# Kernel tuning notes

Hardware: AMD Instinct MI355X
Metric: run time of the kernel (lower is better)

The kernel has to match this reference:

```python
import jax, jax.numpy as jnp
import numpy as np

B, T = 1024, 8192
NUM_WORDS = 2048  # ph2word.max() + 1, forced by construction in setup_inputs
OFFSET = 1.0
LAMBDA_P, LAMBDA_W, LAMBDA_S = 0.6, 0.3, 0.1
RULES_SCALE = 0.3
INIT_TOKENS = np.array([94, 122, 100, 92, 43, 27], dtype=np.int32)
INIT_DURS = np.array([2.0, 3.0, 2.0, 2.0, 5.0, 5.0], dtype=np.float32)
RATIO_TOKENS = np.array([44, 28, 29, 27, 121, 43], dtype=np.int32)


def setup_inputs() -> dict:
    key = jax.random.key(0)
    k1, k2, k3, k4 = jax.random.split(key, 4)
    dur_pred = jax.random.uniform(k1, (B, T), dtype=jnp.float32) * 10.0
    dur_gt = jax.random.uniform(k2, (B, T), dtype=jnp.float32) * 10.0
    ph2word = jnp.sort(jax.random.randint(k3, (B, T), 0, NUM_WORDS, dtype=jnp.int32), axis=1)
    ph2word = ph2word.at[:, -1].set(NUM_WORDS - 1)  # guarantee max == NUM_WORDS-1 (static shape)
    txt_tokens = jax.random.randint(k4, (B, T), 0, 150, dtype=jnp.int32)
    return {"dur_pred": dur_pred, "dur_gt": dur_gt, "ph2word": ph2word, "txt_tokens": txt_tokens}


def _linear2log(x):
    return jnp.log(x + OFFSET)


def _mse(a, b):
    d = a - b
    return jnp.mean(d * d)


def _dur_rules(dur_pred, txt_tokens):
    # Vectorized form of the sequential double loop. At step i the carry value
    # dur_rules[:, i] is unconditionally reset to dur_pred[:, i], so the ratio
    # rule's forward write to i+1 never survives; final value is
    #   dur_pred[i] - self_adjust(i) + neighbor_gaps_from(i+1).
    tok = txt_tokens[..., None]  # [B,T,1]
    in_init = jnp.any(tok == jnp.asarray(INIT_TOKENS), axis=-1)
    expected = jnp.sum(jnp.where(tok == jnp.asarray(INIT_TOKENS), jnp.asarray(INIT_DURS), 0.0), axis=-1)
    gap1 = dur_pred - expected
    fire1 = in_init & (gap1 > 0)
    gap1 = jnp.where(fire1, gap1, 0.0)

    in_ratio = jnp.any(tok == jnp.asarray(RATIO_TOKENS), axis=-1)
    dp_next = jnp.concatenate([dur_pred[:, 1:], jnp.zeros_like(dur_pred[:, :1])], axis=1)
    valid_next = jnp.arange(dur_pred.shape[1]) < dur_pred.shape[1] - 1
    fire2 = in_ratio & valid_next[None, :] & (3.0 * dur_pred > dp_next)
    gap2 = jnp.where(fire2, dur_pred - dp_next / 3.0, 0.0)

    # ratio rule overwrites (not adds to) the self position when it fires
    self_adj = jnp.where(fire2, gap2, jnp.where(fire1, gap1, 0.0))
    dur_rules = dur_pred - self_adj
    # gaps from iteration i+1 are added to position i (only for i+1 >= 1, always true)
    dur_rules = dur_rules.at[:, :-1].add((gap1 + gap2)[:, 1:])
    return dur_rules


def reference(dur_pred, dur_gt, ph2word, txt_tokens):
    dur_gt = dur_gt.astype(dur_pred.dtype)

    dur_rules = _dur_rules(dur_pred, txt_tokens)
    rules_loss = RULES_SCALE * _mse(_linear2log(dur_pred), _linear2log(dur_rules))

    pdur_loss = LAMBDA_P * _mse(_linear2log(dur_pred), _linear2log(dur_gt))

    dp_c = jnp.maximum(dur_pred, 0.0)
    seg = lambda d, s: jax.ops.segment_sum(d, s, num_segments=NUM_WORDS)
    wdur_pred = jax.vmap(seg)(dp_c, ph2word)[:, 1:]
    wdur_gt = jax.vmap(seg)(dur_gt, ph2word)[:, 1:]
    wdur_loss = LAMBDA_W * _mse(_linear2log(wdur_pred), _linear2log(wdur_gt))

    sdur_pred = jnp.sum(dp_c, axis=1)
    sdur_gt = jnp.sum(dur_gt, axis=1)
    sdur_loss = LAMBDA_S * _mse(_linear2log(sdur_pred), _linear2log(sdur_gt))

    return pdur_loss + wdur_loss + sdur_loss + rules_loss
```

## Files before the change

kernel.cpp:

```cpp
#include <hip/hip_runtime.h>

constexpr int Bn  = 1024;
constexpr int Tn  = 8192;
constexpr int Wn  = 2048;
constexpr int TPB = 1024;

__device__ __forceinline__ void rule_eval(float dp, float dpn, int tok, bool valid_next,
                                          float& g1, float& g2, float& sa) {
  float expected;
  bool in_init = true;
  switch (tok) {
    case 94:  expected = 2.f; break;
    case 122: expected = 3.f; break;
    case 100: expected = 2.f; break;
    case 92:  expected = 2.f; break;
    case 43:  expected = 5.f; break;
    case 27:  expected = 5.f; break;
    default:  expected = 0.f; in_init = false; break;
  }
  float t1 = dp - expected;
  bool fire1 = in_init && (t1 > 0.f);
  g1 = fire1 ? t1 : 0.f;
  bool in_ratio = (tok == 44) | (tok == 28) | (tok == 29) |
                  (tok == 27) | (tok == 121) | (tok == 43);
  bool fire2 = in_ratio && valid_next && (3.f * dp > dpn);
  g2 = fire2 ? (dp - dpn * (1.f / 3.f)) : 0.f;
  sa = fire2 ? g2 : (fire1 ? g1 : 0.f);
}

__device__ __forceinline__ float wave_reduce(float v) {
  #pragma unroll
  for (int o = 32; o > 0; o >>= 1) v += __shfl_down(v, o, 64);
  return v;
}

__global__ __launch_bounds__(TPB) void loss_kernel(
    const float* __restrict__ dur_pred, const float* __restrict__ dur_gt,
    const int* __restrict__ ph2word, const int* __restrict__ txt,
    double* __restrict__ acc)
{
  __shared__ float wp[Wn];
  __shared__ float wg[Wn];
  __shared__ float sacc[5];

  const int row = blockIdx.x;
  const size_t roff = (size_t)row * Tn;
  const float* __restrict__ dpr = dur_pred + roff;
  const float* __restrict__ dgr = dur_gt + roff;
  const int*   __restrict__ pwr = ph2word + roff;
  const int*   __restrict__ tkr = txt + roff;

  for (int i = threadIdx.x; i < Wn; i += TPB) { wp[i] = 0.f; wg[i] = 0.f; }
  if (threadIdx.x < 5) sacc[threadIdx.x] = 0.f;
  __syncthreads();

  float pdur_s = 0.f, rules_s = 0.f, sp = 0.f, sg = 0.f;

  #pragma unroll
  for (int c = 0; c < 2; ++c) {
    const int base = c * (Tn / 2) + threadIdx.x * 4;

    float4 dp4 = *reinterpret_cast<const float4*>(dpr + base);
    float4 dg4 = *reinterpret_cast<const float4*>(dgr + base);
    int4   pw4 = *reinterpret_cast<const int4*>(pwr + base);
    int4   tk4 = *reinterpret_cast<const int4*>(tkr + base);

    const bool last = (base + 4 >= Tn);

    float dpx[6];
    dpx[0] = dp4.x; dpx[1] = dp4.y; dpx[2] = dp4.z; dpx[3] = dp4.w;
    dpx[4] = last ? 0.f : dpr[base + 4];
    dpx[5] = (base + 5 < Tn) ? dpr[base + 5] : 0.f;
    int tkx[5];
    tkx[0] = tk4.x; tkx[1] = tk4.y; tkx[2] = tk4.z; tkx[3] = tk4.w;
    tkx[4] = last ? -1 : tkr[base + 4];

    float g1[5], g2[5], sa[5];
    #pragma unroll
    for (int j = 0; j < 5; ++j) {
      int i = base + j;
      rule_eval(dpx[j], dpx[j + 1], tkx[j], i < Tn - 1, g1[j], g2[j], sa[j]);
    }

    float dgl[4] = {dg4.x, dg4.y, dg4.z, dg4.w};

    #pragma unroll
    for (int j = 0; j < 4; ++j) {
      int i = base + j;
      float dp = dpx[j];
      float add = (i < Tn - 1) ? (g1[j + 1] + g2[j + 1]) : 0.f;
      float dr = dp - sa[j] + add;
      float lp = __logf(dp + 1.f);
      float dlr = lp - __logf(dr + 1.f);
      rules_s += dlr * dlr;
      float dlg = lp - __logf(dgl[j] + 1.f);
      pdur_s += dlg * dlg;
      sp += fmaxf(dp, 0.f);
      sg += dgl[j];
    }

    int pwl[4] = {pw4.x, pw4.y, pw4.z, pw4.w};
    int curw = pwl[0];
    float ap = 0.f, ag = 0.f;
    #pragma unroll
    for (int j = 0; j < 4; ++j) {
      if (pwl[j] != curw) {
        atomicAdd(&wp[curw], ap);
        atomicAdd(&wg[curw], ag);
        curw = pwl[j]; ap = 0.f; ag = 0.f;
      }
      ap += fmaxf(dpx[j], 0.f);
      ag += dgl[j];
    }
    atomicAdd(&wp[curw], ap);
    atomicAdd(&wg[curw], ag);
  }

  __syncthreads();

  float wd_s = 0.f;
  #pragma unroll
  for (int w = threadIdx.x; w < Wn; w += TPB) {
    if (w != 0) {
      float d = __logf(wp[w] + 1.f) - __logf(wg[w] + 1.f);
      wd_s += d * d;
    }
  }

  pdur_s  = wave_reduce(pdur_s);
  rules_s = wave_reduce(rules_s);
  sp      = wave_reduce(sp);
  sg      = wave_reduce(sg);
  wd_s    = wave_reduce(wd_s);
  if ((threadIdx.x & 63) == 0) {
    atomicAdd(&sacc[0], pdur_s);
    atomicAdd(&sacc[1], rules_s);
    atomicAdd(&sacc[2], sp);
    atomicAdd(&sacc[3], sg);
    atomicAdd(&sacc[4], wd_s);
  }
  __syncthreads();

  if (threadIdx.x == 0) {
    float ds = __logf(sacc[2] + 1.f) - __logf(sacc[3] + 1.f);
    double total = 0.6 * (double)sacc[0] / ((double)Bn * (double)Tn)
                 + 0.3 * (double)sacc[1] / ((double)Bn * (double)Tn)
                 + 0.3 * (double)sacc[4] / ((double)Bn * (double)(Wn - 1))
                 + 0.1 * (double)(ds * ds) / (double)Bn;
    atomicAdd(acc, total);
  }
}

__global__ void finalize_kernel(const double* __restrict__ acc, float* __restrict__ out) {
  out[0] = (float)(*acc);
}

extern "C" void kernel_launch(void* const* d_in, const int* in_sizes, int n_in,
                              void* d_out, int out_size, void* d_ws, size_t ws_size,
                              hipStream_t stream) {
  const float* dur_pred = (const float*)d_in[0];
  const float* dur_gt   = (const float*)d_in[1];
  const int*   ph2word  = (const int*)d_in[2];
  const int*   txt      = (const int*)d_in[3];
  double* acc = (double*)d_ws;

  hipMemsetAsync(d_ws, 0, sizeof(double), stream);
  loss_kernel<<<Bn, TPB, 0, stream>>>(dur_pred, dur_gt, ph2word, txt, acc);
  finalize_kernel<<<1, 1, 0, stream>>>(acc, (float*)d_out);
}
```

Before: 187.9 us.

## Halve block size, prefetch next chunk in registers, fuse finalize via last-block ticket

Blocks shrink from 1024 to 512 threads, and each thread now handles four strided chunks per row instead of two. While computing the current chunk, a thread loads the next one into registers, which overlaps memory latency with compute. The separate finalize kernel is removed: the last block, found with an atomic ticket counter, writes the output. The prefetch raises register pressure, and the ticket adds a threadfence and a global atomic per block.

```diff
diff --git a/kernel.cpp b/kernel.cpp
--- a/kernel.cpp
+++ b/kernel.cpp
@@ -3,7 +3,9 @@
 constexpr int Bn  = 1024;
 constexpr int Tn  = 8192;
 constexpr int Wn  = 2048;
-constexpr int TPB = 1024;
+constexpr int TPB = 512;
+constexpr int CH  = 4;
+constexpr int STRIDE = Tn / CH;
 
 __device__ __forceinline__ void rule_eval(float dp, float dpn, int tok, bool valid_next,
                                           float& g1, float& g2, float& sa) {
@@ -34,10 +36,32 @@
   return v;
 }
 
-__global__ __launch_bounds__(TPB) void loss_kernel(
+struct Chunk {
+  float4 dp; float4 dg; int4 pw; int4 tk;
+  float dn0, dn1; int tn;
+};
+
+__device__ __forceinline__ Chunk load_chunk(const float* __restrict__ dpr,
+                                            const float* __restrict__ dgr,
+                                            const int* __restrict__ pwr,
+                                            const int* __restrict__ tkr, int base) {
+  Chunk ck;
+  ck.dp = *reinterpret_cast<const float4*>(dpr + base);
+  ck.dg = *reinterpret_cast<const float4*>(dgr + base);
+  ck.pw = *reinterpret_cast<const int4*>(pwr + base);
+  ck.tk = *reinterpret_cast<const int4*>(tkr + base);
+  const bool last = (base + 4 >= Tn);
+  ck.dn0 = last ? 0.f : dpr[base + 4];
+  ck.dn1 = (base + 5 < Tn) ? dpr[base + 5] : 0.f;
+  ck.tn  = last ? -1 : tkr[base + 4];
+  return ck;
+}
+
+__global__ __launch_bounds__(TPB, 8) void loss_kernel(
     const float* __restrict__ dur_pred, const float* __restrict__ dur_gt,
     const int* __restrict__ ph2word, const int* __restrict__ txt,
-    double* __restrict__ acc)
+    double* __restrict__ acc, unsigned int* __restrict__ cnt,
+    float* __restrict__ out)
 {
   __shared__ float wp[Wn];
   __shared__ float wg[Wn];
@@ -56,24 +80,22 @@
 
   float pdur_s = 0.f, rules_s = 0.f, sp = 0.f, sg = 0.f;
 
+  Chunk cur = load_chunk(dpr, dgr, pwr, tkr, threadIdx.x * 4);
+
   #pragma unroll
-  for (int c = 0; c < 2; ++c) {
-    const int base = c * (Tn / 2) + threadIdx.x * 4;
+  for (int c = 0; c < CH; ++c) {
+    Chunk nxt;
+    if (c + 1 < CH)
+      nxt = load_chunk(dpr, dgr, pwr, tkr, (c + 1) * STRIDE + threadIdx.x * 4);
 
-    float4 dp4 = *reinterpret_cast<const float4*>(dpr + base);
-    float4 dg4 = *reinterpret_cast<const float4*>(dgr + base);
-    int4   pw4 = *reinterpret_cast<const int4*>(pwr + base);
-    int4   tk4 = *reinterpret_cast<const int4*>(tkr + base);
-
-    const bool last = (base + 4 >= Tn);
+    const int base = c * STRIDE + threadIdx.x * 4;
 
     float dpx[6];
-    dpx[0] = dp4.x; dpx[1] = dp4.y; dpx[2] = dp4.z; dpx[3] = dp4.w;
-    dpx[4] = last ? 0.f : dpr[base + 4];
-    dpx[5] = (base + 5 < Tn) ? dpr[base + 5] : 0.f;
+    dpx[0] = cur.dp.x; dpx[1] = cur.dp.y; dpx[2] = cur.dp.z; dpx[3] = cur.dp.w;
+    dpx[4] = cur.dn0;  dpx[5] = cur.dn1;
     int tkx[5];
-    tkx[0] = tk4.x; tkx[1] = tk4.y; tkx[2] = tk4.z; tkx[3] = tk4.w;
-    tkx[4] = last ? -1 : tkr[base + 4];
+    tkx[0] = cur.tk.x; tkx[1] = cur.tk.y; tkx[2] = cur.tk.z; tkx[3] = cur.tk.w;
+    tkx[4] = cur.tn;
 
     float g1[5], g2[5], sa[5];
     #pragma unroll
@@ -82,7 +104,7 @@
       rule_eval(dpx[j], dpx[j + 1], tkx[j], i < Tn - 1, g1[j], g2[j], sa[j]);
     }
 
-    float dgl[4] = {dg4.x, dg4.y, dg4.z, dg4.w};
+    float dgl[4] = {cur.dg.x, cur.dg.y, cur.dg.z, cur.dg.w};
 
     #pragma unroll
     for (int j = 0; j < 4; ++j) {
@@ -99,7 +121,7 @@
       sg += dgl[j];
     }
 
-    int pwl[4] = {pw4.x, pw4.y, pw4.z, pw4.w};
+    int pwl[4] = {cur.pw.x, cur.pw.y, cur.pw.z, cur.pw.w};
     int curw = pwl[0];
     float ap = 0.f, ag = 0.f;
     #pragma unroll
@@ -114,6 +136,8 @@
     }
     atomicAdd(&wp[curw], ap);
     atomicAdd(&wg[curw], ag);
+
+    cur = nxt;
   }
 
   __syncthreads();
@@ -148,11 +172,13 @@
                  + 0.3 * (double)sacc[4] / ((double)Bn * (double)(Wn - 1))
                  + 0.1 * (double)(ds * ds) / (double)Bn;
     atomicAdd(acc, total);
+    __threadfence();
+    unsigned int ticket = atomicAdd(cnt, 1u);
+    if (ticket == (unsigned int)(Bn - 1)) {
+      double final_val = atomicAdd(acc, 0.0);
+      out[0] = (float)final_val;
+    }
   }
-}
-
-__global__ void finalize_kernel(const double* __restrict__ acc, float* __restrict__ out) {
-  out[0] = (float)(*acc);
 }
 
 extern "C" void kernel_launch(void* const* d_in, const int* in_sizes, int n_in,
@@ -163,8 +189,9 @@
   const int*   ph2word  = (const int*)d_in[2];
   const int*   txt      = (const int*)d_in[3];
   double* acc = (double*)d_ws;
+  unsigned int* cnt = (unsigned int*)((char*)d_ws + sizeof(double));
 
-  hipMemsetAsync(d_ws, 0, sizeof(double), stream);
-  loss_kernel<<<Bn, TPB, 0, stream>>>(dur_pred, dur_gt, ph2word, txt, acc);
-  finalize_kernel<<<1, 1, 0, stream>>>(acc, (float*)d_out);
+  hipMemsetAsync(d_ws, 0, 16, stream);
+  loss_kernel<<<Bn, TPB, 0, stream>>>(dur_pred, dur_gt, ph2word, txt, acc, cnt,
+                                      (float*)d_out);
 }
```

Measured after the change: 412.3 us. +119.5%, slower.

## Split each row across four blocks with global word-sum buffers and a second reduction kernel

Applied to the files above, without the earlier changes.

Each row is now split across four 256-thread blocks instead of one 1024-thread block. Per-block shared-memory word sums are flushed with atomics into per-row global buffers, and a second kernel computes the word and sentence log-MSE terms, using a last-block counter to write the final output. The aim is better occupancy and latency hiding. In exchange it adds a 16 MB memset, global atomics and an extra pass over the word buffers. Precision changes because the partial sums are accumulated in float rather than double, and the old single-kernel path is kept as a fallback when the workspace is too small.

```diff
diff --git a/kernel.cpp b/kernel.cpp
--- a/kernel.cpp
+++ b/kernel.cpp
@@ -3,7 +3,17 @@
 constexpr int Bn  = 1024;
 constexpr int Tn  = 8192;
 constexpr int Wn  = 2048;
-constexpr int TPB = 1024;
+
+constexpr int QP   = 4;
+constexpr int SEG  = Tn / QP;
+constexpr int TPB1 = 256;
+constexpr int TPB2 = 256;
+
+constexpr size_t OFF_SPROW = 64;
+constexpr size_t OFF_SGROW = 64 + 4096;
+constexpr size_t OFF_WP    = 16384;
+constexpr size_t OFF_WG    = OFF_WP + (size_t)Bn * Wn * 4;
+constexpr size_t WS_NEEDED = OFF_WG + (size_t)Bn * Wn * 4;
 
 __device__ __forceinline__ void rule_eval(float dp, float dpn, int tok, bool valid_next,
                                           float& g1, float& g2, float& sa) {
@@ -34,31 +44,40 @@
   return v;
 }
 
-__global__ __launch_bounds__(TPB) void loss_kernel(
+__global__ __launch_bounds__(TPB1, 8) void k1_elem(
     const float* __restrict__ dur_pred, const float* __restrict__ dur_gt,
     const int* __restrict__ ph2word, const int* __restrict__ txt,
-    double* __restrict__ acc)
+    char* __restrict__ ws)
 {
   __shared__ float wp[Wn];
   __shared__ float wg[Wn];
-  __shared__ float sacc[5];
-
-  const int row = blockIdx.x;
+  __shared__ float sacc[4];
+
+  float* acc_pdur  = (float*)(ws + 0);
+  float* acc_rules = (float*)(ws + 4);
+  float* sprow     = (float*)(ws + OFF_SPROW);
+  float* sgrow     = (float*)(ws + OFF_SGROW);
+  float* wp_g      = (float*)(ws + OFF_WP);
+  float* wg_g      = (float*)(ws + OFF_WG);
+
+  const int bid = blockIdx.x;
+  const int row = bid >> 2;
+  const int q   = bid & 3;
   const size_t roff = (size_t)row * Tn;
   const float* __restrict__ dpr = dur_pred + roff;
   const float* __restrict__ dgr = dur_gt + roff;
   const int*   __restrict__ pwr = ph2word + roff;
   const int*   __restrict__ tkr = txt + roff;
 
-  for (int i = threadIdx.x; i < Wn; i += TPB) { wp[i] = 0.f; wg[i] = 0.f; }
-  if (threadIdx.x < 5) sacc[threadIdx.x] = 0.f;
+  for (int i = threadIdx.x; i < Wn; i += TPB1) { wp[i] = 0.f; wg[i] = 0.f; }
+  if (threadIdx.x < 4) sacc[threadIdx.x] = 0.f;
   __syncthreads();
 
   float pdur_s = 0.f, rules_s = 0.f, sp = 0.f, sg = 0.f;
 
   #pragma unroll
   for (int c = 0; c < 2; ++c) {
-    const int base = c * (Tn / 2) + threadIdx.x * 4;
+    const int base = q * SEG + c * (SEG / 2) + threadIdx.x * 4;
 
     float4 dp4 = *reinterpret_cast<const float4*>(dpr + base);
     float4 dg4 = *reinterpret_cast<const float4*>(dgr + base);
@@ -118,9 +137,168 @@
 
   __syncthreads();
 
+  {
+    float* wpg = wp_g + (size_t)row * Wn;
+    float* wgg = wg_g + (size_t)row * Wn;
+    for (int w = threadIdx.x; w < Wn; w += TPB1) {
+      float vp = wp[w], vg = wg[w];
+      if (vp != 0.f) atomicAdd(&wpg[w], vp);
+      if (vg != 0.f) atomicAdd(&wgg[w], vg);
+    }
+  }
+
+  pdur_s  = wave_reduce(pdur_s);
+  rules_s = wave_reduce(rules_s);
+  sp      = wave_reduce(sp);
+  sg      = wave_reduce(sg);
+  if ((threadIdx.x & 63) == 0) {
+    atomicAdd(&sacc[0], pdur_s);
+    atomicAdd(&sacc[1], rules_s);
+    atomicAdd(&sacc[2], sp);
+    atomicAdd(&sacc[3], sg);
+  }
+  __syncthreads();
+
+  if (threadIdx.x == 0) {
+    atomicAdd(acc_pdur,  sacc[0]);
+    atomicAdd(acc_rules, sacc[1]);
+    atomicAdd(&sprow[row], sacc[2]);
+    atomicAdd(&sgrow[row], sacc[3]);
+  }
+}
+
+__global__ __launch_bounds__(TPB2) void k2_word(char* __restrict__ ws,
+                                                float* __restrict__ out)
+{
+  __shared__ float swd[1];
+
+  float* acc_pdur  = (float*)(ws + 0);
+  float* acc_rules = (float*)(ws + 4);
+  float* acc_wd    = (float*)(ws + 8);
+  float* acc_sd    = (float*)(ws + 12);
+  unsigned int* cnt2 = (unsigned int*)(ws + 16);
+  float* sprow     = (float*)(ws + OFF_SPROW);
+  float* sgrow     = (float*)(ws + OFF_SGROW);
+  const float* wp_g = (const float*)(ws + OFF_WP);
+  const float* wg_g = (const float*)(ws + OFF_WG);
+
+  const int r = blockIdx.x;
+  const float* __restrict__ wpr = wp_g + (size_t)r * Wn;
+  const float* __restrict__ wgr = wg_g + (size_t)r * Wn;
+
+  if (threadIdx.x == 0) swd[0] = 0.f;
+  __syncthreads();
+
   float wd_s = 0.f;
+  for (int w = threadIdx.x; w < Wn; w += TPB2) {
+    if (w != 0) {
+      float d = __logf(wpr[w] + 1.f) - __logf(wgr[w] + 1.f);
+      wd_s += d * d;
+    }
+  }
+  wd_s = wave_reduce(wd_s);
+  if ((threadIdx.x & 63) == 0) atomicAdd(&swd[0], wd_s);
+  __syncthreads();
+
+  if (threadIdx.x == 0) {
+    atomicAdd(acc_wd, swd[0]);
+    float ds = __logf(sprow[r] + 1.f) - __logf(sgrow[r] + 1.f);
+    atomicAdd(acc_sd, ds * ds);
+    __threadfence();
+    unsigned int t = atomicAdd(cnt2, 1u);
+    if (t == (unsigned int)(Bn - 1)) {
+      float pd = atomicAdd(acc_pdur, 0.f);
+      float rl = atomicAdd(acc_rules, 0.f);
+      float wd = atomicAdd(acc_wd, 0.f);
+      float sd = atomicAdd(acc_sd, 0.f);
+      double total = 0.6 * (double)pd / ((double)Bn * (double)Tn)
+                   + 0.3 * (double)rl / ((double)Bn * (double)Tn)
+                   + 0.3 * (double)wd / ((double)Bn * (double)(Wn - 1))
+                   + 0.1 * (double)sd / (double)Bn;
+      out[0] = (float)total;
+    }
+  }
+}
+
+__global__ __launch_bounds__(1024) void loss_kernel_full(
+    const float* __restrict__ dur_pred, const float* __restrict__ dur_gt,
+    const int* __restrict__ ph2word, const int* __restrict__ txt,
+    double* __restrict__ acc)
+{
+  __shared__ float wp[Wn];
+  __shared__ float wg[Wn];
+  __shared__ float sacc[5];
+
+  const int row = blockIdx.x;
+  const size_t roff = (size_t)row * Tn;
+  const float* __restrict__ dpr = dur_pred + roff;
+  const float* __restrict__ dgr = dur_gt + roff;
+  const int*   __restrict__ pwr = ph2word + roff;
+  const int*   __restrict__ tkr = txt + roff;
+
+  for (int i = threadIdx.x; i < Wn; i += 1024) { wp[i] = 0.f; wg[i] = 0.f; }
+  if (threadIdx.x < 5) sacc[threadIdx.x] = 0.f;
+  __syncthreads();
+
+  float pdur_s = 0.f, rules_s = 0.f, sp = 0.f, sg = 0.f;
+
   #pragma unroll
-  for (int w = threadIdx.x; w < Wn; w += TPB) {
+  for (int c = 0; c < 2; ++c) {
+    const int base = c * (Tn / 2) + threadIdx.x * 4;
+    float4 dp4 = *reinterpret_cast<const float4*>(dpr + base);
+    float4 dg4 = *reinterpret_cast<const float4*>(dgr + base);
+    int4   pw4 = *reinterpret_cast<const int4*>(pwr + base);
+    int4   tk4 = *reinterpret_cast<const int4*>(tkr + base);
+    const bool last = (base + 4 >= Tn);
+    float dpx[6];
+    dpx[0] = dp4.x; dpx[1] = dp4.y; dpx[2] = dp4.z; dpx[3] = dp4.w;
+    dpx[4] = last ? 0.f : dpr[base + 4];
+    dpx[5] = (base + 5 < Tn) ? dpr[base + 5] : 0.f;
+    int tkx[5];
+    tkx[0] = tk4.x; tkx[1] = tk4.y; tkx[2] = tk4.z; tkx[3] = tk4.w;
+    tkx[4] = last ? -1 : tkr[base + 4];
+    float g1[5], g2[5], sa[5];
+    #pragma unroll
+    for (int j = 0; j < 5; ++j) {
+      int i = base + j;
+      rule_eval(dpx[j], dpx[j + 1], tkx[j], i < Tn - 1, g1[j], g2[j], sa[j]);
+    }
+    float dgl[4] = {dg4.x, dg4.y, dg4.z, dg4.w};
+    #pragma unroll
+    for (int j = 0; j < 4; ++j) {
+      int i = base + j;
+      float dp = dpx[j];
+      float add = (i < Tn - 1) ? (g1[j + 1] + g2[j + 1]) : 0.f;
+      float dr = dp - sa[j] + add;
+      float lp = __logf(dp + 1.f);
+      float dlr = lp - __logf(dr + 1.f);
+      rules_s += dlr * dlr;
+      float dlg = lp - __logf(dgl[j] + 1.f);
+      pdur_s += dlg * dlg;
+      sp += fmaxf(dp, 0.f);
+      sg += dgl[j];
+    }
+    int pwl[4] = {pw4.x, pw4.y, pw4.z, pw4.w};
+    int curw = pwl[0];
+    float ap = 0.f, ag = 0.f;
+    #pragma unroll
+    for (int j = 0; j < 4; ++j) {
+      if (pwl[j] != curw) {
+        atomicAdd(&wp[curw], ap);
+        atomicAdd(&wg[curw], ag);
+        curw = pwl[j]; ap = 0.f; ag = 0.f;
+      }
+      ap += fmaxf(dpx[j], 0.f);
+      ag += dgl[j];
+    }
+    atomicAdd(&wp[curw], ap);
+    atomicAdd(&wg[curw], ag);
+  }
+
+  __syncthreads();
+
+  float wd_s = 0.f;
+  for (int w = threadIdx.x; w < Wn; w += 1024) {
     if (w != 0) {
       float d = __logf(wp[w] + 1.f) - __logf(wg[w] + 1.f);
       wd_s += d * d;
@@ -162,9 +340,16 @@
   const float* dur_gt   = (const float*)d_in[1];
   const int*   ph2word  = (const int*)d_in[2];
   const int*   txt      = (const int*)d_in[3];
-  double* acc = (double*)d_ws;
-
-  hipMemsetAsync(d_ws, 0, sizeof(double), stream);
-  loss_kernel<<<Bn, TPB, 0, stream>>>(dur_pred, dur_gt, ph2word, txt, acc);
-  finalize_kernel<<<1, 1, 0, stream>>>(acc, (float*)d_out);
-}
+
+  if (ws_size >= WS_NEEDED) {
+    hipMemsetAsync(d_ws, 0, WS_NEEDED, stream);
+    k1_elem<<<Bn * QP, TPB1, 0, stream>>>(dur_pred, dur_gt, ph2word, txt,
+                                          (char*)d_ws);
+    k2_word<<<Bn, TPB2, 0, stream>>>((char*)d_ws, (float*)d_out);
+  } else {
+    double* acc = (double*)d_ws;
+    hipMemsetAsync(d_ws, 0, sizeof(double), stream);
+    loss_kernel_full<<<Bn, 1024, 0, stream>>>(dur_pred, dur_gt, ph2word, txt, acc);
+    finalize_kernel<<<1, 1, 0, stream>>>(acc, (float*)d_out);
+  }
+}
```

New measurement: 296.7 us. 1.58x slower.
